# Performance work log

Hardware: AMD Instinct MI355X
Metric: run time of the kernel (lower is better)

## Reference

```python
import jax, jax.numpy as jnp
import numpy as np
from jax.scipy.special import erf

B, S, D, H, F = 2, 2048, 1024, 16, 4096
EPS = 1e-5


def setup_inputs() -> dict:
    key = jax.random.key(0)
    ks = jax.random.split(key, 7)
    s = 0.02  # init scale so attention logits stay in a sane range
    return {
        "x": jax.random.normal(ks[0], (B, S, D), jnp.float32),
        "wq": jax.random.normal(ks[1], (D, D), jnp.float32) * s,
        "wk": jax.random.normal(ks[2], (D, D), jnp.float32) * s,
        "wv": jax.random.normal(ks[3], (D, D), jnp.float32) * s,
        "wo": jax.random.normal(ks[4], (D, D), jnp.float32) * s,
        "w1": jax.random.normal(ks[5], (F, D), jnp.float32) * s,
        "w2": jax.random.normal(ks[6], (D, F), jnp.float32) * s,
        "g1": jnp.ones((D,), jnp.float32),
        "g2": jnp.ones((D,), jnp.float32),
    }


def _rmsnorm(x, g):
    return x / jnp.sqrt(jnp.mean(x * x, axis=-1, keepdims=True) + EPS) * g


def _gelu_exact(x):
    # 0.5 * x * (1 + erf(x / sqrt(2)))
    return 0.5 * x * (1.0 + erf(x * (1.0 / np.sqrt(2.0).astype(np.float32))))


def reference(x, wq, wk, wv, wo, w1, w2, g1, g2):
    b, s, d = x.shape
    dk = d // H
    # --- attention sublayer (pre-RMSNorm) ---
    h = _rmsnorm(x, g1)
    # Linear(bias=False): y = h @ W.T; split heads -> [b, H, s, dk]
    q = (h @ wq.T).reshape(b, s, H, dk).transpose(0, 2, 1, 3)
    k = (h @ wk.T).reshape(b, s, H, dk).transpose(0, 2, 1, 3)
    v = (h @ wv.T).reshape(b, s, H, dk).transpose(0, 2, 1, 3)
    scores = jnp.einsum('bhqd,bhkd->bhqk', q, k) / jnp.sqrt(jnp.float32(dk))
    causal = jnp.triu(jnp.ones((s, s), bool), 1)  # True above diagonal -> masked
    scores = jnp.where(causal, -jnp.inf, scores)
    attn = jax.nn.softmax(scores, axis=-1)
    o = jnp.einsum('bhqk,bhkd->bhqd', attn, v)
    o = o.transpose(0, 2, 1, 3).reshape(b, s, d) @ wo.T
    x = x + o
    # --- FFN sublayer (pre-RMSNorm, exact-erf GELU) ---
    h2 = _rmsnorm(x, g2)
    f = _gelu_exact(h2 @ w1.T) @ w2.T
    return x + f
```

## Files before the change

kernel.cpp:

```cpp
#include <hip/hip_runtime.h>
#include <hip/hip_bf16.h>
#include <math.h>

#define B_   2
#define S_   2048
#define D_   1024
#define H_   16
#define DK_  64
#define F_   4096
#define NTOK (B_ * S_)

typedef __bf16 bf16x8 __attribute__((ext_vector_type(8)));
typedef float  f32x4  __attribute__((ext_vector_type(4)));

__device__ __forceinline__ unsigned short bf16r(float f) {
  unsigned u = __builtin_bit_cast(unsigned, f);
  u += 0x7fffu + ((u >> 16) & 1u);
  return (unsigned short)(u >> 16);
}

__device__ __forceinline__ void gload_lds16(const void* g, void* l) {
  __builtin_amdgcn_global_load_lds(
      (__attribute__((address_space(1))) void*)g,
      (__attribute__((address_space(3))) void*)l, 16, 0, 0);
}

__device__ __forceinline__ unsigned lds_off(void* p) {
  return (unsigned)(size_t)(__attribute__((address_space(3))) void*)p;
}
__device__ __forceinline__ bf16x8 ds_read16(unsigned a) {
  bf16x8 r;
  asm volatile("ds_read_b128 %0, %1" : "=v"(r) : "v"(a));
  return r;
}
__device__ __forceinline__ void ds_write32(unsigned a, unsigned v) {
  asm volatile("ds_write_b32 %0, %1" : : "v"(a), "v"(v));
}
__device__ __forceinline__ float fexp2(float x) {
  float r;
  asm volatile("v_exp_f32 %0, %1\n\ts_nop 0" : "=v"(r) : "v"(x));
  return r;
}
__device__ __forceinline__ unsigned cvt_pk_bf16(float lo, float hi) {
  unsigned r;
  asm volatile("v_cvt_pk_bf16_f32 %0, %1, %2" : "=v"(r) : "v"(lo), "v"(hi));
  return r;
}

__device__ __forceinline__ float gelu_fast(float x) {
  float y = 0.7978845608f * x * (1.0f + 0.044715f * x * x);
  float e = fexp2(2.885390082f * y);
  float t = 1.0f - 2.0f / (e + 1.0f);
  return 0.5f * x * (1.0f + t);
}

#define QSCL 0.18033688f

struct CvtArgs {
  const float* src[6];
  unsigned short* dst[6];
  int start[7];
};
__global__ __launch_bounds__(256) void cvt_all_kernel(CvtArgs a) {
  int i = blockIdx.x * blockDim.x + threadIdx.x;
  if (i >= a.start[6]) return;
  int k = 0;
#pragma unroll
  for (int j = 1; j < 6; ++j)
    if (i >= a.start[j]) k = j;
  int off = i - a.start[k];
  float4 v = reinterpret_cast<const float4*>(a.src[k])[off];
  ushort4 o;
  o.x = bf16r(v.x); o.y = bf16r(v.y); o.z = bf16r(v.z); o.w = bf16r(v.w);
  reinterpret_cast<ushort4*>(a.dst[k])[off] = o;
}

__global__ __launch_bounds__(256) void rmsnorm_kernel(
    const float* __restrict__ x, const float* __restrict__ g,
    unsigned short* __restrict__ out) {
  int row = blockIdx.x;
  int t = threadIdx.x, lane = t & 63, w = t >> 6;
  float4 v = reinterpret_cast<const float4*>(x + (size_t)row * D_)[t];
  float ss = v.x * v.x + v.y * v.y + v.z * v.z + v.w * v.w;
#pragma unroll
  for (int d = 1; d < 64; d <<= 1) ss += __shfl_xor(ss, d);
  __shared__ float red[4];
  if (lane == 0) red[w] = ss;
  __syncthreads();
  float tot = red[0] + red[1] + red[2] + red[3];
  float rstd = rsqrtf(tot * (1.0f / D_) + 1e-5f);
  float4 gv = reinterpret_cast<const float4*>(g)[t];
  ushort4 o;
  o.x = bf16r(v.x * rstd * gv.x);
  o.y = bf16r(v.y * rstd * gv.y);
  o.z = bf16r(v.z * rstd * gv.z);
  o.w = bf16r(v.w * rstd * gv.w);
  reinterpret_cast<ushort4*>(out + (size_t)row * D_)[t] = o;
}

__global__ __launch_bounds__(256) void skred_kernel(
    const float* __restrict__ pb, const float* __restrict__ resid,
    float* __restrict__ out, int n4) {
  int i = blockIdx.x * blockDim.x + threadIdx.x;
  if (i >= n4) return;
  float4 a = reinterpret_cast<const float4*>(pb)[i];
  float4 b = reinterpret_cast<const float4*>(pb + (size_t)NTOK * D_)[i];
  float4 r = reinterpret_cast<const float4*>(resid)[i];
  float4 o;
  o.x = a.x + b.x + r.x;
  o.y = a.y + b.y + r.y;
  o.z = a.z + b.z + r.z;
  o.w = a.w + b.w + r.w;
  reinterpret_cast<float4*>(out)[i] = o;
}

__global__ __launch_bounds__(512, 4) void ffn1_gemm(
    const unsigned short* __restrict__ A, const unsigned short* __restrict__ Bw,
    int M, int N, int K, unsigned short* __restrict__ outB) {
  constexpr int BUFU = 12288;
  __shared__ __attribute__((aligned(16))) unsigned short lds[3 * BUFU];
  const int t = threadIdx.x, lane = t & 63, w = t >> 6;
  const int wm = w >> 1, wn = w & 1;
  const int lg = lane >> 4, ln = lane & 15;

  const int gx = gridDim.x;
  int bid = blockIdx.y * gx + blockIdx.x;
  int xcd = bid & 7, c = bid >> 3;
  int RX = gx >> 2, RY = gridDim.y >> 1;
  int bx = (xcd & 3) * RX + (c % RX);
  int by = (xcd >> 2) * RY + (c / RX);
  const int m0 = by * 256, n0 = bx * 128;

  const int nt = K >> 5;

  auto stage = [&](int tile) {
    int buf = tile % 3;
    const int k0 = tile << 5;
    unsigned short* la = &lds[buf * BUFU];
    unsigned short* lb = la + 8192;
#pragma unroll
    for (int i = 0; i < 2; ++i) {
      int g = i * 512 + t;
      int Ln = g >> 3, p = g & 7, u = p ^ (Ln & 7);
      int row = 2 * Ln + (u >> 2), cg = u & 3;
      gload_lds16(A + (size_t)(m0 + row) * K + k0 + cg * 8, &la[g * 8]);
    }
    {
      int Ln = t >> 3, p = t & 7, u = p ^ (Ln & 7);
      int row = 2 * Ln + (u >> 2), cg = u & 3;
      gload_lds16(Bw + (size_t)(n0 + row) * K + k0 + cg * 8, &lb[t * 8]);
    }
  };

  stage(0);
  stage(1);

  const unsigned base0 = lds_off(lds);
  unsigned offA[4], offB[4];
#pragma unroll
  for (int m = 0; m < 4; ++m) {
    int r = wm * 64 + m * 16 + ln;
    int Ln = r >> 1, p = ((r & 1) * 4 + lg) ^ (Ln & 7);
    offA[m] = (unsigned)((Ln * 64 + p * 8) * 2);
  }
#pragma unroll
  for (int n = 0; n < 4; ++n) {
    int r = wn * 64 + n * 16 + ln;
    int Ln = r >> 1, p = ((r & 1) * 4 + lg) ^ (Ln & 7);
    offB[n] = (unsigned)(16384 + (Ln * 64 + p * 8) * 2);
  }

  f32x4 acc[4][4] = {};

  for (int tile = 0; tile < nt; ++tile) {
    if (tile + 1 < nt) { asm volatile("s_waitcnt vmcnt(3)"); }
    else               { asm volatile("s_waitcnt vmcnt(0)"); }
    __builtin_amdgcn_sched_barrier(0);
    __builtin_amdgcn_s_barrier();
    const unsigned bb = base0 + (unsigned)((tile % 3) * (BUFU * 2));
    bf16x8 af[4], bf0, bf1;
#pragma unroll
    for (int m = 0; m < 4; ++m) af[m] = ds_read16(bb + offA[m]);
    bf0 = ds_read16(bb + offB[0]);
    bf1 = ds_read16(bb + offB[1]);
    if (tile + 2 < nt) stage(tile + 2);
    asm volatile("s_waitcnt lgkmcnt(0)");
    __builtin_amdgcn_sched_barrier(0);
    __builtin_amdgcn_s_setprio(1);
#pragma unroll
    for (int m = 0; m < 4; ++m) {
      acc[m][0] = __builtin_amdgcn_mfma_f32_16x16x32_bf16(af[m], bf0, acc[m][0], 0, 0, 0);
      acc[m][1] = __builtin_amdgcn_mfma_f32_16x16x32_bf16(af[m], bf1, acc[m][1], 0, 0, 0);
    }
    __builtin_amdgcn_s_setprio(0);
    bf0 = ds_read16(bb + offB[2]);
    bf1 = ds_read16(bb + offB[3]);
    asm volatile("s_waitcnt lgkmcnt(0)");
    __builtin_amdgcn_sched_barrier(0);
    __builtin_amdgcn_s_setprio(1);
#pragma unroll
    for (int m = 0; m < 4; ++m) {
      acc[m][2] = __builtin_amdgcn_mfma_f32_16x16x32_bf16(af[m], bf0, acc[m][2], 0, 0, 0);
      acc[m][3] = __builtin_amdgcn_mfma_f32_16x16x32_bf16(af[m], bf1, acc[m][3], 0, 0, 0);
    }
    __builtin_amdgcn_s_setprio(0);
  }

  const int rbase = m0 + wm * 64 + lg * 4;
  const int cbase = n0 + wn * 64 + ln;
#pragma unroll
  for (int m = 0; m < 4; ++m) {
#pragma unroll
    for (int n = 0; n < 4; ++n) {
      int col = cbase + n * 16;
#pragma unroll
      for (int j = 0; j < 4; ++j) {
        int row = rbase + m * 16 + j;
        outB[(size_t)row * N + col] = bf16r(gelu_fast(acc[m][n][j]));
      }
    }
  }
}

__global__ __launch_bounds__(256, 3) void qkv_gemm(
    const unsigned short* __restrict__ A, const unsigned short* __restrict__ Bw,
    int M, int N, int K,
    unsigned short* __restrict__ outB, unsigned short* __restrict__ outB2,
    unsigned short* __restrict__ outB3) {
  constexpr int BUFU = 8192;
  __shared__ __attribute__((aligned(16))) unsigned short lds[3 * BUFU];
  const int t = threadIdx.x, lane = t & 63, w = t >> 6;
  const int wm = w >> 1, wn = w & 1;
  const int lg = lane >> 4, ln = lane & 15;

  const int gx = gridDim.x;
  int bid = blockIdx.y * gx + blockIdx.x;
  int xcd = bid & 7, c = bid >> 3;
  int RX = gx >> 2, RY = gridDim.y >> 1;
  int bx = (xcd & 3) * RX + (c % RX);
  int by = (xcd >> 2) * RY + (c / RX);
  const int m0 = by * 128, n0 = bx * 128;

  const int nt = K >> 5;

  auto stage = [&](int tile) {
    int buf = tile % 3;
    const int k0 = tile << 5;
    unsigned short* la = &lds[buf * BUFU];
    unsigned short* lb = la + 4096;
#pragma unroll
    for (int i = 0; i < 2; ++i) {
      int g = i * 256 + t;
      int Ln = g >> 3, p = g & 7, u = p ^ (Ln & 7);
      int row = 2 * Ln + (u >> 2), cg = u & 3;
      gload_lds16(A + (size_t)(m0 + row) * K + k0 + cg * 8, &la[g * 8]);
    }
#pragma unroll
    for (int i = 0; i < 2; ++i) {
      int g = i * 256 + t;
      int Ln = g >> 3, p = g & 7, u = p ^ (Ln & 7);
      int row = 2 * Ln + (u >> 2), cg = u & 3;
      gload_lds16(Bw + (size_t)(n0 + row) * K + k0 + cg * 8, &lb[g * 8]);
    }
  };

  stage(0);
  stage(1);

  const unsigned base0 = lds_off(lds);
  unsigned offA[4], offB[4];
#pragma unroll
  for (int m = 0; m < 4; ++m) {
    int r = wm * 64 + m * 16 + ln;
    int Ln = r >> 1, p = ((r & 1) * 4 + lg) ^ (Ln & 7);
    offA[m] = (unsigned)((Ln * 64 + p * 8) * 2);
  }
#pragma unroll
  for (int n = 0; n < 4; ++n) {
    int r = wn * 64 + n * 16 + ln;
    int Ln = r >> 1, p = ((r & 1) * 4 + lg) ^ (Ln & 7);
    offB[n] = (unsigned)(8192 + (Ln * 64 + p * 8) * 2);
  }

  f32x4 acc[4][4] = {};

  for (int tile = 0; tile < nt; ++tile) {
    if (tile + 1 < nt) { asm volatile("s_waitcnt vmcnt(4)"); }
    else               { asm volatile("s_waitcnt vmcnt(0)"); }
    __builtin_amdgcn_sched_barrier(0);
    __builtin_amdgcn_s_barrier();
    const unsigned bb = base0 + (unsigned)((tile % 3) * (BUFU * 2));
    bf16x8 af[4], bf[4];
#pragma unroll
    for (int m = 0; m < 4; ++m) af[m] = ds_read16(bb + offA[m]);
#pragma unroll
    for (int n = 0; n < 4; ++n) bf[n] = ds_read16(bb + offB[n]);
    if (tile + 2 < nt) stage(tile + 2);
    asm volatile("s_waitcnt lgkmcnt(0)");
    __builtin_amdgcn_sched_barrier(0);
    __builtin_amdgcn_s_setprio(1);
#pragma unroll
    for (int m = 0; m < 4; ++m)
#pragma unroll
      for (int n = 0; n < 4; ++n)
        acc[m][n] = __builtin_amdgcn_mfma_f32_16x16x32_bf16(af[m], bf[n], acc[m][n], 0, 0, 0);
    __builtin_amdgcn_s_setprio(0);
  }

  const int rbase = m0 + wm * 64 + lg * 4;
  const int cbase = n0 + wn * 64 + ln;
#pragma unroll
  for (int m = 0; m < 4; ++m) {
#pragma unroll
    for (int n = 0; n < 4; ++n) {
      int col = cbase + n * 16;
#pragma unroll
      for (int j = 0; j < 4; ++j) {
        int row = rbase + m * 16 + j;
        float v = acc[m][n][j];
        if (col < D_) {
          outB[(size_t)row * D_ + col] = bf16r(v * QSCL);
        } else if (col < 2 * D_) {
          outB2[(size_t)row * D_ + (col - D_)] = bf16r(v);
        } else {
          int bb2 = row >> 11, s = row & (S_ - 1);
          outB3[((size_t)(bb2 * D_) + (col - 2 * D_)) * S_ + s] = bf16r(v);
        }
      }
    }
  }
}

template <int SPLITK>
__device__ __forceinline__ void gemm128_body(
    const unsigned short* __restrict__ A, const unsigned short* __restrict__ Bw,
    int M, int N, int K, int koff, int klen,
    const float* __restrict__ resid, float* __restrict__ outF) {
  constexpr int BUFU = 256 * 32;
  __shared__ __attribute__((aligned(16))) unsigned short lds[4 * BUFU];
  const int t = threadIdx.x, lane = t & 63, w = t >> 6;
  const int wm = w >> 2, wn = w & 3;
  const int lg = lane >> 4, ln = lane & 15;

  const int gx = gridDim.x;
  int bid = blockIdx.y * gx + blockIdx.x;
  int RX = gx >> 2, RY = gridDim.y >> 1;
  int xcd = bid & 7, c = bid >> 3;
  int bx = (xcd & 3) * RX + (c % RX);
  int by = (xcd >> 2) * RY + (c / RX);
  const int m0 = by * 128, n0 = bx * 128;

  const int nt = klen >> 5;

  auto stage = [&](int tile) {
    const int buf = tile & 3;
    const int k0 = koff + (tile << 5);
    unsigned short* la = &lds[buf * BUFU];
    unsigned short* lb = la + 4096;
    int Ln = t >> 3, p = t & 7, u = p ^ (Ln & 7);
    int row = 2 * Ln + (u >> 2), cg = u & 3;
    gload_lds16(A + (size_t)(m0 + row) * K + k0 + cg * 8, &la[t * 8]);
    gload_lds16(Bw + (size_t)(n0 + row) * K + k0 + cg * 8, &lb[t * 8]);
  };

  stage(0);
  if (nt > 1) stage(1);
  if (nt > 2) stage(2);

  const unsigned base0 = lds_off(lds);
  unsigned offA[4], offB[2];
#pragma unroll
  for (int m = 0; m < 4; ++m) {
    int r = wm * 64 + m * 16 + ln;
    int Ln = r >> 1, p = ((r & 1) * 4 + lg) ^ (Ln & 7);
    offA[m] = (unsigned)((Ln * 64 + p * 8) * 2);
  }
#pragma unroll
  for (int n = 0; n < 2; ++n) {
    int r = wn * 32 + n * 16 + ln;
    int Ln = r >> 1, p = ((r & 1) * 4 + lg) ^ (Ln & 7);
    offB[n] = (unsigned)(8192 + (Ln * 64 + p * 8) * 2);
  }

  f32x4 acc[4][2] = {};

  for (int tile = 0; tile < nt; ++tile) {
    const int rem = nt - 1 - tile;
    if (rem >= 2)      { asm volatile("s_waitcnt vmcnt(4)"); }
    else if (rem == 1) { asm volatile("s_waitcnt vmcnt(2)"); }
    else               { asm volatile("s_waitcnt vmcnt(0)"); }
    __builtin_amdgcn_sched_barrier(0);
    __builtin_amdgcn_s_barrier();
    const unsigned bb = base0 + (unsigned)((tile & 3) * (BUFU * 2));
    bf16x8 af[4], bf[2];
#pragma unroll
    for (int m = 0; m < 4; ++m) af[m] = ds_read16(bb + offA[m]);
#pragma unroll
    for (int n = 0; n < 2; ++n) bf[n] = ds_read16(bb + offB[n]);
    if (tile + 3 < nt) stage(tile + 3);
    asm volatile("s_waitcnt lgkmcnt(0)");
    __builtin_amdgcn_sched_barrier(0);
    __builtin_amdgcn_s_setprio(1);
#pragma unroll
    for (int m = 0; m < 4; ++m)
#pragma unroll
      for (int n = 0; n < 2; ++n)
        acc[m][n] = __builtin_amdgcn_mfma_f32_16x16x32_bf16(af[m], bf[n], acc[m][n], 0, 0, 0);
    __builtin_amdgcn_s_setprio(0);
  }

  const int rbase = m0 + wm * 64 + lg * 4;
  const int cbase = n0 + wn * 32 + ln;
#pragma unroll
  for (int m = 0; m < 4; ++m) {
#pragma unroll
    for (int n = 0; n < 2; ++n) {
      int col = cbase + n * 16;
#pragma unroll
      for (int j = 0; j < 4; ++j) {
        int row = rbase + m * 16 + j;
        if (SPLITK == 0) {
          outF[(size_t)row * N + col] = acc[m][n][j] + resid[(size_t)row * N + col];
        } else {
          outF[(size_t)row * N + col] = acc[m][n][j];
        }
      }
    }
  }
}

__global__ __launch_bounds__(512, 4) void wo_gemm(
    const unsigned short* __restrict__ A, const unsigned short* __restrict__ Bw,
    int M, int N, int K, const float* __restrict__ resid, float* __restrict__ outF) {
  gemm128_body<0>(A, Bw, M, N, K, 0, K, resid, outF);
}
__global__ __launch_bounds__(512, 4) void ffn2_gemm_sk(
    const unsigned short* __restrict__ A, const unsigned short* __restrict__ Bw,
    int M, int N, int K, float* __restrict__ pb) {
  const int kz = blockIdx.z;
  gemm128_body<1>(A, Bw, M, N, K, kz * (K >> 1), K >> 1, nullptr,
                  pb + (size_t)kz * M * N);
}

__global__ __launch_bounds__(256, 2) void attn_kernel(
    const unsigned short* __restrict__ qg, const unsigned short* __restrict__ kg,
    const unsigned short* __restrict__ vt, unsigned short* __restrict__ og) {
  __shared__ __attribute__((aligned(16))) unsigned short Kl[2][8192];
  __shared__ __attribute__((aligned(16))) unsigned short Vl[2][8192];
  __shared__ __attribute__((aligned(16))) unsigned short Pl[4][2048];
  const int t = threadIdx.x, lane = t & 63, w = t >> 6;
  const int lg = lane >> 4, ln = lane & 15;

  int bid = blockIdx.x;
  int nl = (bid & 7) * 64 + (bid >> 3);
  int bh = nl >> 4, pi = nl & 15;
  int b = bh >> 4, h = bh & 15;

  const unsigned kbase = lds_off(&Kl[0][0]);
  const unsigned vbase = lds_off(&Vl[0][0]);
  const unsigned pbase = lds_off(&Pl[w][0]);

  auto runq = [&](int qtile, bool first) {
    const int q0 = qtile * 64;
    const int qw = q0 + w * 16;
    const int nt = (q0 >> 7) + 1;

    bf16x8 aq[2];
    {
      const unsigned short* qp =
          qg + (size_t)(b * S_ + qw + ln) * D_ + h * DK_ + lg * 8;
      aq[0] = *reinterpret_cast<const bf16x8*>(qp);
      aq[1] = *reinterpret_cast<const bf16x8*>(qp + 32);
    }
    asm volatile("" : : "v"(aq[0]), "v"(aq[1]));

    float mr = -1e30f, lr = 0.f;
    f32x4 oacc[4] = {};

    auto stage = [&](int kt) {
      const int buf = kt & 1;
      const int kv0 = kt * 128;
#pragma unroll
      for (int i = 0; i < 4; ++i) {
        int g = i * 256 + t;
        int row = g >> 3, cg = g & 7, sg = cg ^ (row & 7);
        gload_lds16(kg + (size_t)(b * S_ + kv0 + row) * D_ + h * DK_ + sg * 8,
                    &Kl[buf][g * 8]);
      }
#pragma unroll
      for (int i = 0; i < 4; ++i) {
        int g = i * 256 + t;
        int row = g >> 4, cg = g & 15, sg = cg ^ (row & 15);
        gload_lds16(vt + (size_t)(b * D_ + h * DK_ + row) * S_ + kv0 + sg * 8,
                    &Vl[buf][g * 8]);
      }
    };

    if (!first) __builtin_amdgcn_s_barrier();
    stage(0);

    auto ctile = [&](int kt, bool dm) {
      const unsigned kb = kbase + (unsigned)((kt & 1) * 16384);
      const unsigned vb = vbase + (unsigned)((kt & 1) * 16384);
      f32x4 sc[8] = {};
      bf16x8 kf[8];
#pragma unroll
      for (int n = 0; n < 8; ++n) {
        int r = n * 16 + ln;
        int cg0 = lg ^ (r & 7);
        kf[n] = ds_read16(kb + (unsigned)((r * 128 + cg0 * 16)));
      }
      if (!dm) stage(kt + 1);
      asm volatile("s_waitcnt lgkmcnt(0)");
      __builtin_amdgcn_sched_barrier(0);
#pragma unroll
      for (int n = 0; n < 8; ++n)
        sc[n] = __builtin_amdgcn_mfma_f32_16x16x32_bf16(kf[n], aq[0], sc[n], 0, 0, 0);
#pragma unroll
      for (int n = 0; n < 8; ++n) {
        int r = n * 16 + ln;
        int cg1 = (4 + lg) ^ (r & 7);
        kf[n] = ds_read16(kb + (unsigned)((r * 128 + cg1 * 16)));
      }
      asm volatile("s_waitcnt lgkmcnt(0)");
      __builtin_amdgcn_sched_barrier(0);
#pragma unroll
      for (int n = 0; n < 8; ++n)
        sc[n] = __builtin_amdgcn_mfma_f32_16x16x32_bf16(kf[n], aq[1], sc[n], 0, 0, 0);
      if (dm) {
        const int kv0 = kt * 128;
        const int qi = qw + ln;
#pragma unroll
        for (int n = 0; n < 8; ++n)
#pragma unroll
          for (int j = 0; j < 4; ++j)
            if ((kv0 + n * 16 + lg * 4 + j) > qi) sc[n][j] = -1e30f;
      }
      float mx = -1e30f;
#pragma unroll
      for (int n = 0; n < 8; ++n) {
        float a = fmaxf(fmaxf(sc[n][0], sc[n][1]), fmaxf(sc[n][2], sc[n][3]));
        mx = fmaxf(mx, a);
      }
      mx = fmaxf(mx, __shfl_xor(mx, 16));
      mx = fmaxf(mx, __shfl_xor(mx, 32));
      float mn = fmaxf(mr, mx);
      float ps = 0.f;
#pragma unroll
      for (int n = 0; n < 8; ++n)
#pragma unroll
        for (int j = 0; j < 4; ++j) {
          float p = fexp2(sc[n][j] - mn);
          sc[n][j] = p;
          ps += p;
        }
      if (__all(mx <= mr)) {
        lr += ps;
      } else {
        float sf = fexp2(mr - mn);
        mr = mn;
        lr = lr * sf + ps;
#pragma unroll
        for (int j = 0; j < 4; ++j) {
          float sfj = __shfl(sf, lg * 4 + j);
#pragma unroll
          for (int f = 0; f < 4; ++f) oacc[f][j] *= sfj;
        }
      }
#pragma unroll
      for (int n = 0; n < 8; ++n) {
        int kvc = n * 16 + lg * 4;
        int gsw = ((kvc >> 3) ^ ln) & 15;
        unsigned pa_addr = pbase + (unsigned)(ln * 256 + gsw * 16 + (kvc & 7) * 2);
        ds_write32(pa_addr, cvt_pk_bf16(sc[n][0], sc[n][1]));
        ds_write32(pa_addr + 4, cvt_pk_bf16(sc[n][2], sc[n][3]));
      }
      asm volatile("s_waitcnt lgkmcnt(0)");
      __builtin_amdgcn_sched_barrier(0);
#pragma unroll
      for (int c = 0; c < 4; ++c) {
        unsigned cgp = (unsigned)(((c * 4 + lg) ^ ln) & 15);
        bf16x8 pa = ds_read16(pbase + (unsigned)(ln * 256) + cgp * 16);
        bf16x8 vf[4];
#pragma unroll
        for (int f = 0; f < 4; ++f) {
          int dv = f * 16 + ln;
          int cgv = ((c * 4 + lg) ^ (dv & 15)) & 15;
          vf[f] = ds_read16(vb + (unsigned)(dv * 256 + cgv * 16));
        }
        asm volatile("s_waitcnt lgkmcnt(0)");
        __builtin_amdgcn_sched_barrier(0);
#pragma unroll
        for (int f = 0; f < 4; ++f)
          oacc[f] = __builtin_amdgcn_mfma_f32_16x16x32_bf16(pa, vf[f], oacc[f], 0, 0, 0);
      }
    };

    for (int kt = 0; kt < nt - 1; ++kt) {
      asm volatile("s_waitcnt vmcnt(0)");
      __builtin_amdgcn_sched_barrier(0);
      __builtin_amdgcn_s_barrier();
      ctile(kt, false);
    }
    asm volatile("s_waitcnt vmcnt(0)");
    __builtin_amdgcn_sched_barrier(0);
    __builtin_amdgcn_s_barrier();
    ctile(nt - 1, true);

    lr += __shfl_xor(lr, 16);
    lr += __shfl_xor(lr, 32);
#pragma unroll
    for (int j = 0; j < 4; ++j) {
      float lj = __shfl(lr, lg * 4 + j);
      float inv = 1.0f / lj;
      int row = b * S_ + qw + lg * 4 + j;
#pragma unroll
      for (int f = 0; f < 4; ++f)
        og[(size_t)row * D_ + h * DK_ + f * 16 + ln] = bf16r(oacc[f][j] * inv);
    }
  };

  runq(31 - pi, true);
  runq(pi, false);
}

extern "C" void kernel_launch(void* const* d_in, const int* in_sizes, int n_in,
                              void* d_out, int out_size, void* d_ws, size_t ws_size,
                              hipStream_t stream) {
  const float* x  = (const float*)d_in[0];
  const float* wq = (const float*)d_in[1];
  const float* wk = (const float*)d_in[2];
  const float* wv = (const float*)d_in[3];
  const float* wo = (const float*)d_in[4];
  const float* w1 = (const float*)d_in[5];
  const float* w2 = (const float*)d_in[6];
  const float* g1 = (const float*)d_in[7];
  const float* g2 = (const float*)d_in[8];
  float* out = (float*)d_out;

  char* ws = (char*)d_ws;
  const size_t MB = 1024 * 1024;
  unsigned short* wqkv_b = (unsigned short*)(ws + 0 * MB);
  unsigned short* wo_b   = (unsigned short*)(ws + 6 * MB);
  unsigned short* w1_b   = (unsigned short*)(ws + 8 * MB);
  unsigned short* w2_b   = (unsigned short*)(ws + 16 * MB);
  unsigned short* h_b    = (unsigned short*)(ws + 24 * MB);
  unsigned short* q_b    = (unsigned short*)(ws + 32 * MB);
  unsigned short* k_b    = (unsigned short*)(ws + 40 * MB);
  unsigned short* vt_b   = (unsigned short*)(ws + 48 * MB);
  unsigned short* o_b    = (unsigned short*)(ws + 56 * MB);
  float*          x1     = (float*)(ws + 64 * MB);
  unsigned short* mid    = (unsigned short*)(ws + 80 * MB);
  float*          pb     = (float*)(ws + 24 * MB);

  CvtArgs ca;
  ca.src[0] = wq; ca.dst[0] = wqkv_b;
  ca.src[1] = wk; ca.dst[1] = wqkv_b + (size_t)D_ * D_;
  ca.src[2] = wv; ca.dst[2] = wqkv_b + (size_t)2 * D_ * D_;
  ca.src[3] = wo; ca.dst[3] = wo_b;
  ca.src[4] = w1; ca.dst[4] = w1_b;
  ca.src[5] = w2; ca.dst[5] = w2_b;
  int q4 = D_ * D_ / 4, f4 = F_ * D_ / 4;
  ca.start[0] = 0;
  ca.start[1] = q4;
  ca.start[2] = 2 * q4;
  ca.start[3] = 3 * q4;
  ca.start[4] = 4 * q4;
  ca.start[5] = 4 * q4 + f4;
  ca.start[6] = 4 * q4 + 2 * f4;
  cvt_all_kernel<<<(ca.start[6] + 255) / 256, 256, 0, stream>>>(ca);

  rmsnorm_kernel<<<NTOK, 256, 0, stream>>>(x, g1, h_b);

  qkv_gemm<<<dim3(3 * D_ / 128, NTOK / 128), dim3(256), 0, stream>>>(
      h_b, wqkv_b, NTOK, 3 * D_, D_, q_b, k_b, vt_b);

  attn_kernel<<<dim3(512), dim3(256), 0, stream>>>(q_b, k_b, vt_b, o_b);

  wo_gemm<<<dim3(D_ / 128, NTOK / 128), dim3(512), 0, stream>>>(
      o_b, wo_b, NTOK, D_, D_, x, x1);

  rmsnorm_kernel<<<NTOK, 256, 0, stream>>>(x1, g2, h_b);

  ffn1_gemm<<<dim3(F_ / 128, NTOK / 256), dim3(512), 0, stream>>>(
      h_b, w1_b, NTOK, F_, D_, mid);

  ffn2_gemm_sk<<<dim3(D_ / 128, NTOK / 128, 2), dim3(512), 0, stream>>>(
      mid, w2_b, NTOK, D_, F_, pb);

  skred_kernel<<<(NTOK * D_ / 4 + 255) / 256, 256, 0, stream>>>(
      pb, x1, out, NTOK * D_ / 4);
}
```

Measured before the change: 230.9 us.

## Drop FFN2 split-K with fused residual; software-pipeline attention LDS reads

The FFN2 GEMM no longer splits K across two partial buffers followed by a separate reduction kernel. It now runs a single full-K GEMM that adds the residual in its epilogue, which removes the partial-buffer traffic and one launch but halves the grid (256 blocks). In attention, both K-fragment halves are loaded before the first MFMAs, waiting with partial lgkmcnt counts. The PV loop is double-buffered so LDS reads for the next chunk overlap the current MFMAs, at the cost of more live registers.

```diff
diff --git a/kernel.cpp b/kernel.cpp
--- a/kernel.cpp
+++ b/kernel.cpp
@@ -98,22 +98,6 @@
   reinterpret_cast<ushort4*>(out + (size_t)row * D_)[t] = o;
 }
 
-__global__ __launch_bounds__(256) void skred_kernel(
-    const float* __restrict__ pb, const float* __restrict__ resid,
-    float* __restrict__ out, int n4) {
-  int i = blockIdx.x * blockDim.x + threadIdx.x;
-  if (i >= n4) return;
-  float4 a = reinterpret_cast<const float4*>(pb)[i];
-  float4 b = reinterpret_cast<const float4*>(pb + (size_t)NTOK * D_)[i];
-  float4 r = reinterpret_cast<const float4*>(resid)[i];
-  float4 o;
-  o.x = a.x + b.x + r.x;
-  o.y = a.y + b.y + r.y;
-  o.z = a.z + b.z + r.z;
-  o.w = a.w + b.w + r.w;
-  reinterpret_cast<float4*>(out)[i] = o;
-}
-
 __global__ __launch_bounds__(512, 4) void ffn1_gemm(
     const unsigned short* __restrict__ A, const unsigned short* __restrict__ Bw,
     int M, int N, int K, unsigned short* __restrict__ outB) {
@@ -331,10 +315,9 @@
   }
 }
 
-template <int SPLITK>
 __device__ __forceinline__ void gemm128_body(
     const unsigned short* __restrict__ A, const unsigned short* __restrict__ Bw,
-    int M, int N, int K, int koff, int klen,
+    int M, int N, int K,
     const float* __restrict__ resid, float* __restrict__ outF) {
   constexpr int BUFU = 256 * 32;
   __shared__ __attribute__((aligned(16))) unsigned short lds[4 * BUFU];
@@ -350,11 +333,11 @@
   int by = (xcd >> 2) * RY + (c / RX);
   const int m0 = by * 128, n0 = bx * 128;
 
-  const int nt = klen >> 5;
+  const int nt = K >> 5;
 
   auto stage = [&](int tile) {
     const int buf = tile & 3;
-    const int k0 = koff + (tile << 5);
+    const int k0 = tile << 5;
     unsigned short* la = &lds[buf * BUFU];
     unsigned short* lb = la + 4096;
     int Ln = t >> 3, p = t & 7, u = p ^ (Ln & 7);
@@ -419,11 +402,7 @@
 #pragma unroll
       for (int j = 0; j < 4; ++j) {
         int row = rbase + m * 16 + j;
-        if (SPLITK == 0) {
-          outF[(size_t)row * N + col] = acc[m][n][j] + resid[(size_t)row * N + col];
-        } else {
-          outF[(size_t)row * N + col] = acc[m][n][j];
-        }
+        outF[(size_t)row * N + col] = acc[m][n][j] + resid[(size_t)row * N + col];
       }
     }
   }
@@ -432,15 +411,29 @@
 __global__ __launch_bounds__(512, 4) void wo_gemm(
     const unsigned short* __restrict__ A, const unsigned short* __restrict__ Bw,
     int M, int N, int K, const float* __restrict__ resid, float* __restrict__ outF) {
-  gemm128_body<0>(A, Bw, M, N, K, 0, K, resid, outF);
-}
-__global__ __launch_bounds__(512, 4) void ffn2_gemm_sk(
+  gemm128_body(A, Bw, M, N, K, resid, outF);
+}
+__global__ __launch_bounds__(512, 4) void ffn2_gemm(
     const unsigned short* __restrict__ A, const unsigned short* __restrict__ Bw,
-    int M, int N, int K, float* __restrict__ pb) {
-  const int kz = blockIdx.z;
-  gemm128_body<1>(A, Bw, M, N, K, kz * (K >> 1), K >> 1, nullptr,
-                  pb + (size_t)kz * M * N);
-}
+    int M, int N, int K, const float* __restrict__ resid, float* __restrict__ outF) {
+  gemm128_body(A, Bw, M, N, K, resid, outF);
+}
+
+#define PV_ISSUE(c, pa, v0, v1, v2, v3) do {                                   \
+  unsigned cg_ = (unsigned)(((((c) * 4) + lg) ^ ln) & 15);                     \
+  pa = ds_read16(pbase + (unsigned)(ln * 256) + cg_ * 16);                     \
+  v0 = ds_read16(vb + (unsigned)((0 * 16 + ln) * 256) + cg_ * 16);             \
+  v1 = ds_read16(vb + (unsigned)((1 * 16 + ln) * 256) + cg_ * 16);             \
+  v2 = ds_read16(vb + (unsigned)((2 * 16 + ln) * 256) + cg_ * 16);             \
+  v3 = ds_read16(vb + (unsigned)((3 * 16 + ln) * 256) + cg_ * 16);             \
+} while (0)
+
+#define PV_MFMA(pa, v0, v1, v2, v3) do {                                       \
+  oacc[0] = __builtin_amdgcn_mfma_f32_16x16x32_bf16(pa, v0, oacc[0], 0, 0, 0); \
+  oacc[1] = __builtin_amdgcn_mfma_f32_16x16x32_bf16(pa, v1, oacc[1], 0, 0, 0); \
+  oacc[2] = __builtin_amdgcn_mfma_f32_16x16x32_bf16(pa, v2, oacc[2], 0, 0, 0); \
+  oacc[3] = __builtin_amdgcn_mfma_f32_16x16x32_bf16(pa, v3, oacc[3], 0, 0, 0); \
+} while (0)
 
 __global__ __launch_bounds__(256, 2) void attn_kernel(
     const unsigned short* __restrict__ qg, const unsigned short* __restrict__ kg,
@@ -503,30 +496,30 @@
       const unsigned kb = kbase + (unsigned)((kt & 1) * 16384);
       const unsigned vb = vbase + (unsigned)((kt & 1) * 16384);
       f32x4 sc[8] = {};
-      bf16x8 kf[8];
+      bf16x8 kf[8], kf2[8];
 #pragma unroll
       for (int n = 0; n < 8; ++n) {
         int r = n * 16 + ln;
         int cg0 = lg ^ (r & 7);
         kf[n] = ds_read16(kb + (unsigned)((r * 128 + cg0 * 16)));
       }
-      if (!dm) stage(kt + 1);
-      asm volatile("s_waitcnt lgkmcnt(0)");
-      __builtin_amdgcn_sched_barrier(0);
-#pragma unroll
-      for (int n = 0; n < 8; ++n)
-        sc[n] = __builtin_amdgcn_mfma_f32_16x16x32_bf16(kf[n], aq[0], sc[n], 0, 0, 0);
 #pragma unroll
       for (int n = 0; n < 8; ++n) {
         int r = n * 16 + ln;
         int cg1 = (4 + lg) ^ (r & 7);
-        kf[n] = ds_read16(kb + (unsigned)((r * 128 + cg1 * 16)));
-      }
+        kf2[n] = ds_read16(kb + (unsigned)((r * 128 + cg1 * 16)));
+      }
+      if (!dm) stage(kt + 1);
+      asm volatile("s_waitcnt lgkmcnt(8)");
+      __builtin_amdgcn_sched_barrier(0);
+#pragma unroll
+      for (int n = 0; n < 8; ++n)
+        sc[n] = __builtin_amdgcn_mfma_f32_16x16x32_bf16(kf[n], aq[0], sc[n], 0, 0, 0);
       asm volatile("s_waitcnt lgkmcnt(0)");
       __builtin_amdgcn_sched_barrier(0);
 #pragma unroll
       for (int n = 0; n < 8; ++n)
-        sc[n] = __builtin_amdgcn_mfma_f32_16x16x32_bf16(kf[n], aq[1], sc[n], 0, 0, 0);
+        sc[n] = __builtin_amdgcn_mfma_f32_16x16x32_bf16(kf2[n], aq[1], sc[n], 0, 0, 0);
       if (dm) {
         const int kv0 = kt * 128;
         const int qi = qw + ln;
@@ -577,23 +570,23 @@
       }
       asm volatile("s_waitcnt lgkmcnt(0)");
       __builtin_amdgcn_sched_barrier(0);
-#pragma unroll
-      for (int c = 0; c < 4; ++c) {
-        unsigned cgp = (unsigned)(((c * 4 + lg) ^ ln) & 15);
-        bf16x8 pa = ds_read16(pbase + (unsigned)(ln * 256) + cgp * 16);
-        bf16x8 vf[4];
-#pragma unroll
-        for (int f = 0; f < 4; ++f) {
-          int dv = f * 16 + ln;
-          int cgv = ((c * 4 + lg) ^ (dv & 15)) & 15;
-          vf[f] = ds_read16(vb + (unsigned)(dv * 256 + cgv * 16));
-        }
-        asm volatile("s_waitcnt lgkmcnt(0)");
-        __builtin_amdgcn_sched_barrier(0);
-#pragma unroll
-        for (int f = 0; f < 4; ++f)
-          oacc[f] = __builtin_amdgcn_mfma_f32_16x16x32_bf16(pa, vf[f], oacc[f], 0, 0, 0);
-      }
+      bf16x8 paA, vA0, vA1, vA2, vA3, paB, vB0, vB1, vB2, vB3;
+      PV_ISSUE(0, paA, vA0, vA1, vA2, vA3);
+      PV_ISSUE(1, paB, vB0, vB1, vB2, vB3);
+      asm volatile("s_waitcnt lgkmcnt(5)");
+      __builtin_amdgcn_sched_barrier(0);
+      PV_MFMA(paA, vA0, vA1, vA2, vA3);
+      PV_ISSUE(2, paA, vA0, vA1, vA2, vA3);
+      asm volatile("s_waitcnt lgkmcnt(5)");
+      __builtin_amdgcn_sched_barrier(0);
+      PV_MFMA(paB, vB0, vB1, vB2, vB3);
+      PV_ISSUE(3, paB, vB0, vB1, vB2, vB3);
+      asm volatile("s_waitcnt lgkmcnt(5)");
+      __builtin_amdgcn_sched_barrier(0);
+      PV_MFMA(paA, vA0, vA1, vA2, vA3);
+      asm volatile("s_waitcnt lgkmcnt(0)");
+      __builtin_amdgcn_sched_barrier(0);
+      PV_MFMA(paB, vB0, vB1, vB2, vB3);
     };
 
     for (int kt = 0; kt < nt - 1; ++kt) {
@@ -651,7 +644,6 @@
   unsigned short* o_b    = (unsigned short*)(ws + 56 * MB);
   float*          x1     = (float*)(ws + 64 * MB);
   unsigned short* mid    = (unsigned short*)(ws + 80 * MB);
-  float*          pb     = (float*)(ws + 24 * MB);
 
   CvtArgs ca;
   ca.src[0] = wq; ca.dst[0] = wqkv_b;
@@ -685,9 +677,6 @@
   ffn1_gemm<<<dim3(F_ / 128, NTOK / 256), dim3(512), 0, stream>>>(
       h_b, w1_b, NTOK, F_, D_, mid);
 
-  ffn2_gemm_sk<<<dim3(D_ / 128, NTOK / 128, 2), dim3(512), 0, stream>>>(
-      mid, w2_b, NTOK, D_, F_, pb);
-
-  skred_kernel<<<(NTOK * D_ / 4 + 255) / 256, 256, 0, stream>>>(
-      pb, x1, out, NTOK * D_ / 4);
-}
+  ffn2_gemm<<<dim3(D_ / 128, NTOK / 128), dim3(512), 0, stream>>>(
+      mid, w2_b, NTOK, D_, F_, x1, out);
+}
```

Result: faster. 219.8 us (-4.8%).
